# Kernel optimization log

Measured on AMD Instinct MI355X. Metric: run time of the kernel, lower is better.

Reference implementation:

```python
import jax, jax.numpy as jnp
import numpy as np

N = 50000

def _add_self_loops(edge_index, n):
    loop = jnp.arange(n, dtype=edge_index.dtype)
    src = jnp.concatenate([edge_index[0], loop])
    dst = jnp.concatenate([edge_index[1], loop])
    return src, dst

def _gcn_layer(x, src, dst, norm, W, b, n):
    h = x @ W                                  # [N, out]
    msg = h[src] * norm[:, None]               # [E+N, out] gather + scale
    out = jax.ops.segment_sum(msg, dst, num_segments=n)  # scatter-add
    return out + b

def _gcn_norm(src, dst, n):
    # symmetric normalization D^-1/2 (A+I) D^-1/2 (PyG GCNConv default)
    deg = jax.ops.segment_sum(jnp.ones_like(dst, dtype=jnp.float32), dst, num_segments=n)
    dinv = jnp.where(deg > 0, jax.lax.rsqrt(jnp.maximum(deg, 1.0)), 0.0)
    return dinv[src] * dinv[dst]

def setup_inputs() -> dict:
    key = jax.random.key(0)
    ks = jax.random.split(key, 4)
    x = jax.random.normal(ks[0], (N, 64), dtype=jnp.float32)
    edge_index = jax.random.randint(ks[1], (2, 800000), 0, N, dtype=jnp.int64)
    W1 = jax.random.normal(ks[2], (64, 128), dtype=jnp.float32) * (1.0 / np.sqrt(64))
    b1 = jnp.zeros((128,), dtype=jnp.float32)
    W2 = jax.random.normal(ks[3], (128, 64), dtype=jnp.float32) * (1.0 / np.sqrt(128))
    b2 = jnp.zeros((64,), dtype=jnp.float32)
    return {"x": x, "edge_index": edge_index, "W1": W1, "b1": b1, "W2": W2, "b2": b2}

def reference(x, edge_index, W1, b1, W2, b2):
    n = x.shape[0]
    src, dst = _add_self_loops(edge_index, n)
    norm = _gcn_norm(src, dst, n)
    h = _gcn_layer(x, src, dst, norm, W1, b1, n)
    h = jax.nn.relu(h)
    # dropout with p=0 (eval) is identity
    h = _gcn_layer(h, src, dst, norm, W2, b2, n)
    return jax.nn.relu(h)
```

## Files before the change

### kernel.cpp

```cpp
#include <hip/hip_runtime.h>
#include <hip/hip_fp16.h>
#include <cstddef>
#include <cstdint>

static inline int divup(int a, int b) { return (a + b - 1) / b; }

#define CAP 64
#define EPB 4096
#define BSH 8

__global__ __launch_bounds__(256) void k_bin(const int* __restrict__ src,
                                             const int* __restrict__ dst,
                                             int2* __restrict__ staging,
                                             int* __restrict__ runoff,
                                             int* __restrict__ runlen,
                                             int E, int nbuck, int NB) {
    __shared__ int hist[256];
    __shared__ int scan[256];
    const int t = threadIdx.x;
    const int blk = blockIdx.x;
    const int e0 = blk * EPB;

    int2 ed[16];
    int cb[16];
    #pragma unroll
    for (int j = 0; j < 16; ++j) {
        int idx = e0 + j * 256 + t;
        if (idx < E) {
            ed[j].x = src[idx];
            ed[j].y = dst[idx];
            cb[j] = ed[j].y >> BSH;
        } else {
            cb[j] = -1;
        }
    }
    hist[t] = 0;
    __syncthreads();
    #pragma unroll
    for (int j = 0; j < 16; ++j)
        if (cb[j] >= 0) atomicAdd(&hist[cb[j]], 1);
    __syncthreads();
    scan[t] = hist[t];
    __syncthreads();
    for (int d = 1; d < 256; d <<= 1) {
        int v = (t >= d) ? scan[t - d] : 0;
        __syncthreads();
        scan[t] += v;
        __syncthreads();
    }
    int base = scan[t] - hist[t];
    if (t < nbuck) {
        runoff[t * NB + blk] = base;
        runlen[t * NB + blk] = hist[t];
    }
    hist[t] = base;
    __syncthreads();
    #pragma unroll
    for (int j = 0; j < 16; ++j) {
        if (cb[j] >= 0) {
            int p = atomicAdd(&hist[cb[j]], 1);
            staging[e0 + p] = ed[j];
        }
    }
}

__global__ __launch_bounds__(256) void k_build(const int2* __restrict__ staging,
                                               const int* __restrict__ runoff,
                                               const int* __restrict__ runlen,
                                               const float* __restrict__ x,
                                               int* __restrict__ eidx,
                                               int* __restrict__ cnt,
                                               float* __restrict__ dinv,
                                               __half* __restrict__ xh,
                                               int n, int NB) {
    __shared__ int runstart[512 + 1];
    __shared__ int runbase[512];
    __shared__ int cnt_l[256];
    __shared__ float sdinv[256];
    const int t = threadIdx.x;
    const int b = blockIdx.x;
    const int node0 = b << BSH;

    for (int r = t; r < NB; r += 256) {
        runbase[r] = runoff[b * NB + r];
        runstart[r] = runlen[b * NB + r];
    }
    cnt_l[t] = 0;
    __syncthreads();
    if (t == 0) {
        int run = 0;
        for (int r = 0; r < NB; ++r) { int l = runstart[r]; runstart[r] = run; run += l; }
        runstart[NB] = run;
    }
    __syncthreads();
    const int L = runstart[NB];
    for (int i = t; i < L; i += 256) {
        int lo = 0, hi = NB - 1;
        while (lo < hi) { int mid = (lo + hi + 1) >> 1; if (runstart[mid] <= i) lo = mid; else hi = mid - 1; }
        int2 ed = staging[lo * EPB + runbase[lo] + (i - runstart[lo])];
        int p = atomicAdd(&cnt_l[ed.y - node0], 1);
        if (p < CAP) eidx[(size_t)ed.y * CAP + p] = ed.x;
    }
    __syncthreads();
    int node = node0 + t;
    float di_t = rsqrtf((float)(cnt_l[t] + 1));
    sdinv[t] = di_t;
    if (node < n) {
        cnt[node] = cnt_l[t];
        dinv[node] = di_t;
    }
    __syncthreads();
    for (int i = t; i < 256 * 16; i += 256) {
        int lr = i >> 4, c4 = (i & 15) * 4;
        int nd = node0 + lr;
        if (nd < n) {
            float4 v = *reinterpret_cast<const float4*>(x + (size_t)nd * 64 + c4);
            float di = sdinv[lr];
            __half2 h0 = __floats2half2_rn(v.x * di, v.y * di);
            __half2 h1 = __floats2half2_rn(v.z * di, v.w * di);
            *reinterpret_cast<__half2*>(xh + (size_t)nd * 64 + c4)     = h0;
            *reinterpret_cast<__half2*>(xh + (size_t)nd * 64 + c4 + 2) = h1;
        }
    }
}

__device__ inline void acc8(uint4 u, float a[8]) {
    float2 f0 = __half22float2(*reinterpret_cast<const __half2*>(&u.x));
    float2 f1 = __half22float2(*reinterpret_cast<const __half2*>(&u.y));
    float2 f2 = __half22float2(*reinterpret_cast<const __half2*>(&u.z));
    float2 f3 = __half22float2(*reinterpret_cast<const __half2*>(&u.w));
    a[0] += f0.x; a[1] += f0.y; a[2] += f1.x; a[3] += f1.y;
    a[4] += f2.x; a[5] += f2.y; a[6] += f3.x; a[7] += f3.y;
}

template <bool FINAL>
__global__ __launch_bounds__(256) void k_aggh(const int* __restrict__ cnt,
                                              const int* __restrict__ eidx,
                                              const __half* __restrict__ in16,
                                              const float* __restrict__ dinv,
                                              const float* __restrict__ bias,
                                              float* __restrict__ out64, int n) {
    int t = blockIdx.x * blockDim.x + threadIdx.x;
    int node = t >> 3;
    if (node >= n) return;
    int lane = t & 7;
    const int hoff = lane * 8;
    float a[8] = {0.f, 0.f, 0.f, 0.f, 0.f, 0.f, 0.f, 0.f};
    acc8(*reinterpret_cast<const uint4*>(in16 + (size_t)node * 64 + hoff), a);
    const int b = node * CAP;
    const int eN = b + min(cnt[node], CAP);
    int e = b;
    for (; e + 4 <= eN; e += 4) {
        int s0 = __builtin_nontemporal_load(eidx + e);
        int s1 = __builtin_nontemporal_load(eidx + e + 1);
        int s2 = __builtin_nontemporal_load(eidx + e + 2);
        int s3 = __builtin_nontemporal_load(eidx + e + 3);
        uint4 u0 = *reinterpret_cast<const uint4*>(in16 + (size_t)s0 * 64 + hoff);
        uint4 u1 = *reinterpret_cast<const uint4*>(in16 + (size_t)s1 * 64 + hoff);
        uint4 u2 = *reinterpret_cast<const uint4*>(in16 + (size_t)s2 * 64 + hoff);
        uint4 u3 = *reinterpret_cast<const uint4*>(in16 + (size_t)s3 * 64 + hoff);
        acc8(u0, a); acc8(u1, a); acc8(u2, a); acc8(u3, a);
    }
    for (; e < eN; ++e) {
        int s = __builtin_nontemporal_load(eidx + e);
        acc8(*reinterpret_cast<const uint4*>(in16 + (size_t)s * 64 + hoff), a);
    }
    float di = dinv[node];
    float4 r0, r1;
    r0.x = a[0] * di; r0.y = a[1] * di; r0.z = a[2] * di; r0.w = a[3] * di;
    r1.x = a[4] * di; r1.y = a[5] * di; r1.z = a[6] * di; r1.w = a[7] * di;
    if (FINAL) {
        const float4 b0 = *reinterpret_cast<const float4*>(bias + hoff);
        const float4 b1 = *reinterpret_cast<const float4*>(bias + hoff + 4);
        r0.x = fmaxf(r0.x + b0.x, 0.f); r0.y = fmaxf(r0.y + b0.y, 0.f);
        r0.z = fmaxf(r0.z + b0.z, 0.f); r0.w = fmaxf(r0.w + b0.w, 0.f);
        r1.x = fmaxf(r1.x + b1.x, 0.f); r1.y = fmaxf(r1.y + b1.y, 0.f);
        r1.z = fmaxf(r1.z + b1.z, 0.f); r1.w = fmaxf(r1.w + b1.w, 0.f);
    }
    *reinterpret_cast<float4*>(out64 + (size_t)node * 64 + hoff)     = r0;
    *reinterpret_cast<float4*>(out64 + (size_t)node * 64 + hoff + 4) = r1;
}

__global__ __launch_bounds__(256) void k_gemm1(const float* __restrict__ ax,
                                               const float* __restrict__ W1,
                                               const float* __restrict__ b1,
                                               float* __restrict__ h1f, int n) {
    __shared__ float sA[64][64];
    __shared__ float sW[64][128];
    const int t = threadIdx.x;
    const int r0 = blockIdx.x * 64;
    for (int i = t; i < 64 * 32; i += 256) {
        int k = i >> 5, c4 = (i & 31) * 4;
        *reinterpret_cast<float4*>(&sW[k][c4]) = *reinterpret_cast<const float4*>(W1 + k * 128 + c4);
    }
    for (int i = t; i < 64 * 16; i += 256) {
        int row = i & 63, kq = i >> 6;
        int gr = r0 + row;
        float4 v = {0.f, 0.f, 0.f, 0.f};
        if (gr < n) v = *reinterpret_cast<const float4*>(ax + (size_t)gr * 64 + kq * 4);
        sA[kq * 4 + 0][row] = v.x; sA[kq * 4 + 1][row] = v.y;
        sA[kq * 4 + 2][row] = v.z; sA[kq * 4 + 3][row] = v.w;
    }
    __syncthreads();
    const int tx = t & 15, ty = t >> 4;
    float acc[4][8] = {};
    #pragma unroll 8
    for (int k = 0; k < 64; ++k) {
        float4 a4 = *reinterpret_cast<const float4*>(&sA[k][ty * 4]);
        float4 w0 = *reinterpret_cast<const float4*>(&sW[k][tx * 4]);
        float4 w1 = *reinterpret_cast<const float4*>(&sW[k][64 + tx * 4]);
        float av[4] = {a4.x, a4.y, a4.z, a4.w};
        float wv[8] = {w0.x, w0.y, w0.z, w0.w, w1.x, w1.y, w1.z, w1.w};
        #pragma unroll
        for (int r = 0; r < 4; ++r)
            #pragma unroll
            for (int c = 0; c < 8; ++c)
                acc[r][c] = fmaf(av[r], wv[c], acc[r][c]);
    }
    const float4 bb0 = *reinterpret_cast<const float4*>(b1 + tx * 4);
    const float4 bb1 = *reinterpret_cast<const float4*>(b1 + 64 + tx * 4);
    #pragma unroll
    for (int r = 0; r < 4; ++r) {
        int row = r0 + ty * 4 + r;
        if (row < n) {
            float4 o0 = {fmaxf(acc[r][0] + bb0.x, 0.f), fmaxf(acc[r][1] + bb0.y, 0.f),
                         fmaxf(acc[r][2] + bb0.z, 0.f), fmaxf(acc[r][3] + bb0.w, 0.f)};
            float4 o1 = {fmaxf(acc[r][4] + bb1.x, 0.f), fmaxf(acc[r][5] + bb1.y, 0.f),
                         fmaxf(acc[r][6] + bb1.z, 0.f), fmaxf(acc[r][7] + bb1.w, 0.f)};
            *reinterpret_cast<float4*>(h1f + (size_t)row * 128 + tx * 4)      = o0;
            *reinterpret_cast<float4*>(h1f + (size_t)row * 128 + 64 + tx * 4) = o1;
        }
    }
}

__global__ __launch_bounds__(256) void k_gemm2(const float* __restrict__ h1f,
                                               const float* __restrict__ W2,
                                               const float* __restrict__ dinv,
                                               __half* __restrict__ hs2h, int n) {
    __shared__ float sA[128][64];
    __shared__ float sW[128][64];
    const int t = threadIdx.x;
    const int r0 = blockIdx.x * 64;
    for (int i = t; i < 128 * 16; i += 256) {
        int k = i >> 4, c4 = (i & 15) * 4;
        *reinterpret_cast<float4*>(&sW[k][c4]) = *reinterpret_cast<const float4*>(W2 + k * 64 + c4);
    }
    for (int i = t; i < 64 * 32; i += 256) {
        int row = i & 63, kq = i >> 6;
        int gr = r0 + row;
        float4 v = {0.f, 0.f, 0.f, 0.f};
        if (gr < n) v = *reinterpret_cast<const float4*>(h1f + (size_t)gr * 128 + kq * 4);
        sA[kq * 4 + 0][row] = v.x; sA[kq * 4 + 1][row] = v.y;
        sA[kq * 4 + 2][row] = v.z; sA[kq * 4 + 3][row] = v.w;
    }
    __syncthreads();
    const int tx = t & 15, ty = t >> 4;
    float acc[4][4] = {};
    #pragma unroll 8
    for (int k = 0; k < 128; ++k) {
        float4 a4 = *reinterpret_cast<const float4*>(&sA[k][ty * 4]);
        float4 w4 = *reinterpret_cast<const float4*>(&sW[k][tx * 4]);
        float av[4] = {a4.x, a4.y, a4.z, a4.w};
        float wv[4] = {w4.x, w4.y, w4.z, w4.w};
        #pragma unroll
        for (int r = 0; r < 4; ++r)
            #pragma unroll
            for (int c = 0; c < 4; ++c)
                acc[r][c] = fmaf(av[r], wv[c], acc[r][c]);
    }
    #pragma unroll
    for (int r = 0; r < 4; ++r) {
        int row = r0 + ty * 4 + r;
        if (row < n) {
            float di = dinv[row];
            __half2 h0 = __floats2half2_rn(acc[r][0] * di, acc[r][1] * di);
            __half2 h1 = __floats2half2_rn(acc[r][2] * di, acc[r][3] * di);
            *reinterpret_cast<__half2*>(hs2h + (size_t)row * 64 + tx * 4)     = h0;
            *reinterpret_cast<__half2*>(hs2h + (size_t)row * 64 + tx * 4 + 2) = h1;
        }
    }
}

extern "C" void kernel_launch(void* const* d_in, const int* in_sizes, int n_in,
                              void* d_out, int out_size, void* d_ws, size_t ws_size,
                              hipStream_t stream) {
    const float* x  = (const float*)d_in[0];
    const int*   ei = (const int*)d_in[1];
    const float* W1 = (const float*)d_in[2];
    const float* b1 = (const float*)d_in[3];
    const float* W2 = (const float*)d_in[4];
    const float* b2 = (const float*)d_in[5];
    float* out = (float*)d_out;

    const int n = in_sizes[0] / 64;
    const int E = in_sizes[1] / 2;
    const int* src = ei;
    const int* dst = ei + E;

    const int NB = divup(E, EPB);
    const int nbuck = divup(n, 1 << BSH);

    char* ws = (char*)d_ws;
    size_t off = 0;
    auto alloc = [&](size_t bytes) { void* p = ws + off; off = (off + bytes + 255) & ~(size_t)255; return p; };
    int*    cnt     = (int*)   alloc((size_t)n * 4);
    float*  dinv    = (float*) alloc((size_t)n * 4);
    int2*   staging = (int2*)  alloc((size_t)NB * EPB * 8);
    int*    runoff  = (int*)   alloc((size_t)nbuck * NB * 4);
    int*    runlen  = (int*)   alloc((size_t)nbuck * NB * 4);
    int*    eidx    = (int*)   alloc((size_t)n * CAP * 4);
    __half* xh      = (__half*)alloc((size_t)n * 64 * 2);
    float*  ax      = (float*) alloc((size_t)n * 64 * 4);
    float*  h1f     = (float*) alloc((size_t)n * 128 * 4);
    __half* hs2h    = xh;

    k_bin  <<<NB, 256, 0, stream>>>(src, dst, staging, runoff, runlen, E, nbuck, NB);
    k_build<<<nbuck, 256, 0, stream>>>(staging, runoff, runlen, x, eidx, cnt, dinv, xh, n, NB);

    k_aggh<false><<<divup(n * 8, 256), 256, 0, stream>>>(cnt, eidx, xh, dinv, nullptr, ax, n);
    k_gemm1<<<divup(n, 64), 256, 0, stream>>>(ax, W1, b1, h1f, n);

    k_gemm2<<<divup(n, 64), 256, 0, stream>>>(h1f, W2, dinv, hs2h, n);
    k_aggh<true><<<divup(n * 8, 256), 256, 0, stream>>>(cnt, eidx, hs2h, dinv, b2, out, n);
}
```

Measured before the change: 124.4 us.

## Fuse both dense GEMMs into one fp16 dot2 MLP kernel with fp16 intermediates

The two per-layer GEMM kernels are merged into a single kernel that keeps the 128-wide hidden activation in shared memory as packed fp16, so the fp32 h1f buffer is never written to or read from global memory. The first aggregation now writes its output as fp16 rather than fp32, halving that traffic. A small kernel pre-packs W1 and W2 into half2 pairs along K so the inner loops can use the fdot2 instruction. The cost is lower precision in the GEMM inputs and the hidden activations, plus an extra launch for the weight conversion.

New measurement: 117.2 us. 5.8% less time.

```diff
diff --git a/kernel.cpp b/kernel.cpp
--- a/kernel.cpp
+++ b/kernel.cpp
@@ -8,6 +8,20 @@
 #define CAP 64
 #define EPB 4096
 #define BSH 8
+
+typedef _Float16 h2v __attribute__((ext_vector_type(2)));
+
+__device__ inline float fdot2f(unsigned int a, unsigned int b, float c) {
+#if __has_builtin(__builtin_amdgcn_fdot2)
+    return __builtin_amdgcn_fdot2(__builtin_bit_cast(h2v, a),
+                                  __builtin_bit_cast(h2v, b), c, false);
+#else
+    __half2 ha = __builtin_bit_cast(__half2, a);
+    __half2 hb = __builtin_bit_cast(__half2, b);
+    float2 fa = __half22float2(ha), fb = __half22float2(hb);
+    return fmaf(fa.y, fb.y, fmaf(fa.x, fb.x, c));
+#endif
+}
 
 __global__ __launch_bounds__(256) void k_bin(const int* __restrict__ src,
                                              const int* __restrict__ dst,
@@ -139,7 +153,7 @@
                                               const __half* __restrict__ in16,
                                               const float* __restrict__ dinv,
                                               const float* __restrict__ bias,
-                                              float* __restrict__ out64, int n) {
+                                              void* __restrict__ outp, int n) {
     int t = blockIdx.x * blockDim.x + threadIdx.x;
     int node = t >> 3;
     if (node >= n) return;
@@ -166,117 +180,129 @@
         acc8(*reinterpret_cast<const uint4*>(in16 + (size_t)s * 64 + hoff), a);
     }
     float di = dinv[node];
-    float4 r0, r1;
-    r0.x = a[0] * di; r0.y = a[1] * di; r0.z = a[2] * di; r0.w = a[3] * di;
-    r1.x = a[4] * di; r1.y = a[5] * di; r1.z = a[6] * di; r1.w = a[7] * di;
     if (FINAL) {
+        float* out64 = (float*)outp;
+        float4 r0, r1;
         const float4 b0 = *reinterpret_cast<const float4*>(bias + hoff);
         const float4 b1 = *reinterpret_cast<const float4*>(bias + hoff + 4);
-        r0.x = fmaxf(r0.x + b0.x, 0.f); r0.y = fmaxf(r0.y + b0.y, 0.f);
-        r0.z = fmaxf(r0.z + b0.z, 0.f); r0.w = fmaxf(r0.w + b0.w, 0.f);
-        r1.x = fmaxf(r1.x + b1.x, 0.f); r1.y = fmaxf(r1.y + b1.y, 0.f);
-        r1.z = fmaxf(r1.z + b1.z, 0.f); r1.w = fmaxf(r1.w + b1.w, 0.f);
-    }
-    *reinterpret_cast<float4*>(out64 + (size_t)node * 64 + hoff)     = r0;
-    *reinterpret_cast<float4*>(out64 + (size_t)node * 64 + hoff + 4) = r1;
-}
-
-__global__ __launch_bounds__(256) void k_gemm1(const float* __restrict__ ax,
-                                               const float* __restrict__ W1,
-                                               const float* __restrict__ b1,
-                                               float* __restrict__ h1f, int n) {
-    __shared__ float sA[64][64];
-    __shared__ float sW[64][128];
+        r0.x = fmaxf(fmaf(a[0], di, b0.x), 0.f); r0.y = fmaxf(fmaf(a[1], di, b0.y), 0.f);
+        r0.z = fmaxf(fmaf(a[2], di, b0.z), 0.f); r0.w = fmaxf(fmaf(a[3], di, b0.w), 0.f);
+        r1.x = fmaxf(fmaf(a[4], di, b1.x), 0.f); r1.y = fmaxf(fmaf(a[5], di, b1.y), 0.f);
+        r1.z = fmaxf(fmaf(a[6], di, b1.z), 0.f); r1.w = fmaxf(fmaf(a[7], di, b1.w), 0.f);
+        *reinterpret_cast<float4*>(out64 + (size_t)node * 64 + hoff)     = r0;
+        *reinterpret_cast<float4*>(out64 + (size_t)node * 64 + hoff + 4) = r1;
+    } else {
+        unsigned int* out16 = (unsigned int*)outp;
+        __half2 p0 = __floats2half2_rn(a[0] * di, a[1] * di);
+        __half2 p1 = __floats2half2_rn(a[2] * di, a[3] * di);
+        __half2 p2 = __floats2half2_rn(a[4] * di, a[5] * di);
+        __half2 p3 = __floats2half2_rn(a[6] * di, a[7] * di);
+        uint4 o;
+        o.x = __builtin_bit_cast(unsigned int, p0);
+        o.y = __builtin_bit_cast(unsigned int, p1);
+        o.z = __builtin_bit_cast(unsigned int, p2);
+        o.w = __builtin_bit_cast(unsigned int, p3);
+        *reinterpret_cast<uint4*>(out16 + (size_t)node * 32 + lane * 4) = o;
+    }
+}
+
+__global__ void k_wconv(const float* __restrict__ W1, const float* __restrict__ W2,
+                        unsigned int* __restrict__ w1p, unsigned int* __restrict__ w2p) {
+    int i = blockIdx.x * blockDim.x + threadIdx.x;
+    if (i < 32 * 128) {
+        int kp = i >> 7, c = i & 127;
+        __half2 h = __floats2half2_rn(W1[(size_t)(2 * kp) * 128 + c], W1[(size_t)(2 * kp + 1) * 128 + c]);
+        w1p[i] = __builtin_bit_cast(unsigned int, h);
+    } else if (i < 32 * 128 + 64 * 64) {
+        int j = i - 32 * 128;
+        int kp = j >> 6, c = j & 63;
+        __half2 h = __floats2half2_rn(W2[(size_t)(2 * kp) * 64 + c], W2[(size_t)(2 * kp + 1) * 64 + c]);
+        w2p[j] = __builtin_bit_cast(unsigned int, h);
+    }
+}
+
+__global__ __launch_bounds__(256) void k_mlp(const __half* __restrict__ axh,
+                                             const unsigned int* __restrict__ w1p,
+                                             const unsigned int* __restrict__ w2p,
+                                             const float* __restrict__ b1,
+                                             const float* __restrict__ dinv,
+                                             __half* __restrict__ hs2h, int n) {
+    __shared__ unsigned int sW1[32 * 128];
+    __shared__ unsigned int sW2[64 * 64];
+    __shared__ unsigned int sA[32 * 68];
+    __shared__ unsigned int sH[64 * 68];
     const int t = threadIdx.x;
     const int r0 = blockIdx.x * 64;
-    for (int i = t; i < 64 * 32; i += 256) {
-        int k = i >> 5, c4 = (i & 31) * 4;
-        *reinterpret_cast<float4*>(&sW[k][c4]) = *reinterpret_cast<const float4*>(W1 + k * 128 + c4);
-    }
-    for (int i = t; i < 64 * 16; i += 256) {
-        int row = i & 63, kq = i >> 6;
+    {
+        uint4* d1 = reinterpret_cast<uint4*>(sW1);
+        const uint4* s1 = reinterpret_cast<const uint4*>(w1p);
+        for (int i = t; i < 1024; i += 256) d1[i] = s1[i];
+        uint4* d2 = reinterpret_cast<uint4*>(sW2);
+        const uint4* s2 = reinterpret_cast<const uint4*>(w2p);
+        for (int i = t; i < 1024; i += 256) d2[i] = s2[i];
+    }
+    const unsigned int* axu = reinterpret_cast<const unsigned int*>(axh);
+    for (int i = t; i < 2048; i += 256) {
+        int row = i >> 5, kp = i & 31;
         int gr = r0 + row;
-        float4 v = {0.f, 0.f, 0.f, 0.f};
-        if (gr < n) v = *reinterpret_cast<const float4*>(ax + (size_t)gr * 64 + kq * 4);
-        sA[kq * 4 + 0][row] = v.x; sA[kq * 4 + 1][row] = v.y;
-        sA[kq * 4 + 2][row] = v.z; sA[kq * 4 + 3][row] = v.w;
+        sA[kp * 68 + row] = (gr < n) ? axu[(size_t)gr * 32 + kp] : 0u;
     }
     __syncthreads();
     const int tx = t & 15, ty = t >> 4;
     float acc[4][8] = {};
     #pragma unroll 8
-    for (int k = 0; k < 64; ++k) {
-        float4 a4 = *reinterpret_cast<const float4*>(&sA[k][ty * 4]);
-        float4 w0 = *reinterpret_cast<const float4*>(&sW[k][tx * 4]);
-        float4 w1 = *reinterpret_cast<const float4*>(&sW[k][64 + tx * 4]);
-        float av[4] = {a4.x, a4.y, a4.z, a4.w};
-        float wv[8] = {w0.x, w0.y, w0.z, w0.w, w1.x, w1.y, w1.z, w1.w};
+    for (int kp = 0; kp < 32; ++kp) {
+        uint4 a4 = *reinterpret_cast<const uint4*>(&sA[kp * 68 + ty * 4]);
+        uint4 wA = *reinterpret_cast<const uint4*>(&sW1[kp * 128 + tx * 4]);
+        uint4 wB = *reinterpret_cast<const uint4*>(&sW1[kp * 128 + 64 + tx * 4]);
+        unsigned int av[4] = {a4.x, a4.y, a4.z, a4.w};
+        unsigned int wv[8] = {wA.x, wA.y, wA.z, wA.w, wB.x, wB.y, wB.z, wB.w};
         #pragma unroll
         for (int r = 0; r < 4; ++r)
             #pragma unroll
             for (int c = 0; c < 8; ++c)
-                acc[r][c] = fmaf(av[r], wv[c], acc[r][c]);
+                acc[r][c] = fdot2f(av[r], wv[c], acc[r][c]);
     }
     const float4 bb0 = *reinterpret_cast<const float4*>(b1 + tx * 4);
     const float4 bb1 = *reinterpret_cast<const float4*>(b1 + 64 + tx * 4);
     #pragma unroll
     for (int r = 0; r < 4; ++r) {
-        int row = r0 + ty * 4 + r;
-        if (row < n) {
-            float4 o0 = {fmaxf(acc[r][0] + bb0.x, 0.f), fmaxf(acc[r][1] + bb0.y, 0.f),
-                         fmaxf(acc[r][2] + bb0.z, 0.f), fmaxf(acc[r][3] + bb0.w, 0.f)};
-            float4 o1 = {fmaxf(acc[r][4] + bb1.x, 0.f), fmaxf(acc[r][5] + bb1.y, 0.f),
-                         fmaxf(acc[r][6] + bb1.z, 0.f), fmaxf(acc[r][7] + bb1.w, 0.f)};
-            *reinterpret_cast<float4*>(h1f + (size_t)row * 128 + tx * 4)      = o0;
-            *reinterpret_cast<float4*>(h1f + (size_t)row * 128 + 64 + tx * 4) = o1;
-        }
-    }
-}
-
-__global__ __launch_bounds__(256) void k_gemm2(const float* __restrict__ h1f,
-                                               const float* __restrict__ W2,
-                                               const float* __restrict__ dinv,
-                                               __half* __restrict__ hs2h, int n) {
-    __shared__ float sA[128][64];
-    __shared__ float sW[128][64];
-    const int t = threadIdx.x;
-    const int r0 = blockIdx.x * 64;
-    for (int i = t; i < 128 * 16; i += 256) {
-        int k = i >> 4, c4 = (i & 15) * 4;
-        *reinterpret_cast<float4*>(&sW[k][c4]) = *reinterpret_cast<const float4*>(W2 + k * 64 + c4);
-    }
-    for (int i = t; i < 64 * 32; i += 256) {
-        int row = i & 63, kq = i >> 6;
-        int gr = r0 + row;
-        float4 v = {0.f, 0.f, 0.f, 0.f};
-        if (gr < n) v = *reinterpret_cast<const float4*>(h1f + (size_t)gr * 128 + kq * 4);
-        sA[kq * 4 + 0][row] = v.x; sA[kq * 4 + 1][row] = v.y;
-        sA[kq * 4 + 2][row] = v.z; sA[kq * 4 + 3][row] = v.w;
-    }
-    __syncthreads();
-    const int tx = t & 15, ty = t >> 4;
-    float acc[4][4] = {};
+        int row = ty * 4 + r;
+        float h0 = fmaxf(acc[r][0] + bb0.x, 0.f), h1 = fmaxf(acc[r][1] + bb0.y, 0.f);
+        float h2 = fmaxf(acc[r][2] + bb0.z, 0.f), h3 = fmaxf(acc[r][3] + bb0.w, 0.f);
+        float h4 = fmaxf(acc[r][4] + bb1.x, 0.f), h5 = fmaxf(acc[r][5] + bb1.y, 0.f);
+        float h6 = fmaxf(acc[r][6] + bb1.z, 0.f), h7 = fmaxf(acc[r][7] + bb1.w, 0.f);
+        __half2 p;
+        p = __floats2half2_rn(h0, h1); sH[(2 * tx + 0) * 68 + row]  = __builtin_bit_cast(unsigned int, p);
+        p = __floats2half2_rn(h2, h3); sH[(2 * tx + 1) * 68 + row]  = __builtin_bit_cast(unsigned int, p);
+        p = __floats2half2_rn(h4, h5); sH[(32 + 2 * tx) * 68 + row] = __builtin_bit_cast(unsigned int, p);
+        p = __floats2half2_rn(h6, h7); sH[(33 + 2 * tx) * 68 + row] = __builtin_bit_cast(unsigned int, p);
+    }
+    __syncthreads();
+    float acc2[4][4] = {};
     #pragma unroll 8
-    for (int k = 0; k < 128; ++k) {
-        float4 a4 = *reinterpret_cast<const float4*>(&sA[k][ty * 4]);
-        float4 w4 = *reinterpret_cast<const float4*>(&sW[k][tx * 4]);
-        float av[4] = {a4.x, a4.y, a4.z, a4.w};
-        float wv[4] = {w4.x, w4.y, w4.z, w4.w};
+    for (int kp = 0; kp < 64; ++kp) {
+        uint4 a4 = *reinterpret_cast<const uint4*>(&sH[kp * 68 + ty * 4]);
+        uint4 w4 = *reinterpret_cast<const uint4*>(&sW2[kp * 64 + tx * 4]);
+        unsigned int av[4] = {a4.x, a4.y, a4.z, a4.w};
+        unsigned int wv[4] = {w4.x, w4.y, w4.z, w4.w};
         #pragma unroll
         for (int r = 0; r < 4; ++r)
             #pragma unroll
             for (int c = 0; c < 4; ++c)
-                acc[r][c] = fmaf(av[r], wv[c], acc[r][c]);
+                acc2[r][c] = fdot2f(av[r], wv[c], acc2[r][c]);
     }
     #pragma unroll
     for (int r = 0; r < 4; ++r) {
         int row = r0 + ty * 4 + r;
         if (row < n) {
             float di = dinv[row];
-            __half2 h0 = __floats2half2_rn(acc[r][0] * di, acc[r][1] * di);
-            __half2 h1 = __floats2half2_rn(acc[r][2] * di, acc[r][3] * di);
-            *reinterpret_cast<__half2*>(hs2h + (size_t)row * 64 + tx * 4)     = h0;
-            *reinterpret_cast<__half2*>(hs2h + (size_t)row * 64 + tx * 4 + 2) = h1;
+            __half2 q0 = __floats2half2_rn(acc2[r][0] * di, acc2[r][1] * di);
+            __half2 q1 = __floats2half2_rn(acc2[r][2] * di, acc2[r][3] * di);
+            uint2 o;
+            o.x = __builtin_bit_cast(unsigned int, q0);
+            o.y = __builtin_bit_cast(unsigned int, q1);
+            *reinterpret_cast<uint2*>(hs2h + (size_t)row * 64 + tx * 4) = o;
         }
     }
 }
@@ -310,16 +336,18 @@
     int*    runlen  = (int*)   alloc((size_t)nbuck * NB * 4);
     int*    eidx    = (int*)   alloc((size_t)n * CAP * 4);
     __half* xh      = (__half*)alloc((size_t)n * 64 * 2);
-    float*  ax      = (float*) alloc((size_t)n * 64 * 4);
-    float*  h1f     = (float*) alloc((size_t)n * 128 * 4);
+    __half* axh     = (__half*)alloc((size_t)n * 64 * 2);
+    unsigned int* w1p = (unsigned int*)alloc(32 * 128 * 4);
+    unsigned int* w2p = (unsigned int*)alloc(64 * 64 * 4);
     __half* hs2h    = xh;
 
     k_bin  <<<NB, 256, 0, stream>>>(src, dst, staging, runoff, runlen, E, nbuck, NB);
     k_build<<<nbuck, 256, 0, stream>>>(staging, runoff, runlen, x, eidx, cnt, dinv, xh, n, NB);
-
-    k_aggh<false><<<divup(n * 8, 256), 256, 0, stream>>>(cnt, eidx, xh, dinv, nullptr, ax, n);
-    k_gemm1<<<divup(n, 64), 256, 0, stream>>>(ax, W1, b1, h1f, n);
-
-    k_gemm2<<<divup(n, 64), 256, 0, stream>>>(h1f, W2, dinv, hs2h, n);
+    k_wconv<<<32, 256, 0, stream>>>(W1, W2, w1p, w2p);
+
+    k_aggh<false><<<divup(n * 8, 256), 256, 0, stream>>>(cnt, eidx, xh, dinv, nullptr, axh, n);
+
+    k_mlp<<<divup(n, 64), 256, 0, stream>>>(axh, w1p, w2p, b1, dinv, hs2h, n);
+
     k_aggh<true><<<divup(n * 8, 256), 256, 0, stream>>>(cnt, eidx, hs2h, dinv, b2, out, n);
 }
```
